# Kernel optimization log

Measured on AMD Instinct MI355X. Metric: run time of the kernel, lower is better.

Reference implementation:

```python
import jax, jax.numpy as jnp
import numpy as np

OUT_FEATURES = 4096
IN_FEATURES = 4096
GROUP_SIZE = 16


def setup_inputs() -> dict:
    key = jax.random.key(0)
    k1, k2, k3, k4 = jax.random.split(key, 4)
    n_groups = OUT_FEATURES * IN_FEATURES // GROUP_SIZE
    x = jax.random.normal(k1, (8, 2048, IN_FEATURES), dtype=jnp.float32)
    weight_q = jax.random.randint(k2, (n_groups, GROUP_SIZE), 0, 16, dtype=jnp.int32).astype(jnp.int8)
    weight_norm = jax.random.uniform(k3, (n_groups, 1), dtype=jnp.float32).astype(jnp.float16)
    bias = jax.random.normal(k4, (OUT_FEATURES,), dtype=jnp.float32)
    return {"x": x, "weight_q": weight_q, "weight_norm": weight_norm, "bias": bias}


def reference(x, weight_q, weight_norm, bias):
    # block dequant: (q/15) * per-group scale, then reshape to [out, in]
    w = (weight_q.astype(jnp.float32) / 15.0) * weight_norm.astype(jnp.float32)
    w = w.reshape(OUT_FEATURES, IN_FEATURES)
    # F.linear: x @ w^T + bias
    return jnp.einsum('bsi,oi->bso', x, w) + bias
```

## Files before the change

### kernel.cpp

```cpp
#include <hip/hip_runtime.h>

#define MDIM 16384
#define NDIM 4096
#define KDIM 4096
#define NT   64

typedef unsigned short u16;
typedef unsigned int   u32;
typedef __attribute__((ext_vector_type(8))) short bh8;
typedef __attribute__((ext_vector_type(4))) float f32x4;
typedef __attribute__((ext_vector_type(4))) int   i32x4;

__device__ __forceinline__ u16 f2bf(float f) {
  u32 u = __builtin_bit_cast(u32, f);
  u = (u + 0x7fffu + ((u >> 16) & 1u)) >> 16;
  return (u16)u;
}

__device__ __forceinline__ void gld16(const void* g, const void* lds) {
  __builtin_amdgcn_global_load_lds((const __attribute__((address_space(1))) u32*)g,
                                   (__attribute__((address_space(3))) u32*)lds, 16, 0, 0);
}

__global__ void cvt_x(const float* __restrict__ x, u16* __restrict__ xb) {
  size_t i = ((size_t)blockIdx.x * 256 + threadIdx.x) * 8;
  f32x4 a = *(const f32x4*)(x + i);
  f32x4 b = *(const f32x4*)(x + i + 4);
  bh8 o;
  o[0] = (short)f2bf(a[0]); o[1] = (short)f2bf(a[1]);
  o[2] = (short)f2bf(a[2]); o[3] = (short)f2bf(a[3]);
  o[4] = (short)f2bf(b[0]); o[5] = (short)f2bf(b[1]);
  o[6] = (short)f2bf(b[2]); o[7] = (short)f2bf(b[3]);
  *(bh8*)(xb + i) = o;
}

__global__ void deq_w(const int* __restrict__ qi, const void* __restrict__ nrm,
                      u16* __restrict__ wb) {
  __shared__ int s_q8, s_n32;
  if (threadIdx.x == 0) {
    int packed = 0;
    for (int t = 0; t < 64; ++t) { unsigned v = (unsigned)qi[t]; if (v > 15u) packed = 1; }
    int n32 = 0;
    const u16* h = (const u16*)nrm;
    for (int t = 0; t < 64; ++t) { u16 b = h[t]; if (b < 0x8000u && b > 0x3C00u) n32 = 1; }
    s_q8 = packed; s_n32 = n32;
  }
  __syncthreads();
  const bool q8 = (s_q8 != 0), n32 = (s_n32 != 0);

  int g = blockIdx.x * 256 + threadIdx.x;
  float s;
  if (n32) s = ((const float*)nrm)[g] * (1.0f / 15.0f);
  else {
    u16 hb = ((const u16*)nrm)[g];
    s = (float)__builtin_bit_cast(_Float16, hb) * (1.0f / 15.0f);
  }
  float q[16];
  if (q8) {
    i32x4 v = *(const i32x4*)((const unsigned char*)qi + (size_t)g * 16);
#pragma unroll
    for (int k = 0; k < 4; ++k) {
      int word = v[k];
      q[k*4+0] = (float)(word & 255);        q[k*4+1] = (float)((word >> 8) & 255);
      q[k*4+2] = (float)((word >> 16) & 255); q[k*4+3] = (float)((word >> 24) & 255);
    }
  } else {
    const i32x4* p = (const i32x4*)(qi + (size_t)g * 16);
#pragma unroll
    for (int k = 0; k < 4; ++k) {
      i32x4 v = p[k];
      q[k*4+0] = (float)v[0]; q[k*4+1] = (float)v[1];
      q[k*4+2] = (float)v[2]; q[k*4+3] = (float)v[3];
    }
  }
  bh8 o0, o1;
#pragma unroll
  for (int j = 0; j < 8; ++j) o0[j] = (short)f2bf(q[j] * s);
#pragma unroll
  for (int j = 0; j < 8; ++j) o1[j] = (short)f2bf(q[8 + j] * s);
  *(bh8*)(wb + (size_t)g * 16) = o0;
  *(bh8*)(wb + (size_t)g * 16 + 8) = o1;
}

__global__ __launch_bounds__(512, 2) void gemm8(const u16* __restrict__ A,
                                                const u16* __restrict__ B,
                                                const float* __restrict__ bias,
                                                float* __restrict__ out) {
  __shared__ u16 lds[65536];
  const int tid = threadIdx.x;
  const int w = tid >> 6, l = tid & 63;
  const int wm = w >> 2, wn = w & 3;

  int bid = blockIdx.x;
  int wg = (bid & 7) * 128 + (bid >> 3);
  const int bm = wg >> 4;
  const int bn = wg & 15;

  const int cs8  = ((l & 7) ^ (l >> 3)) * 8;
  const u16* aSrc = A + (size_t)(bm * 256 + w * 32 + (l >> 3)) * 4096 + cs8;
  const u16* bSrc = B + (size_t)(bn * 256 + w * 32 + (l >> 3)) * 4096 + cs8;

  const int fr  = (l & 15) * 64;
  const int sz0 = ((l >> 4) ^ (l & 7)) * 8;
  const int sz1 = ((4 + (l >> 4)) ^ (l & 7)) * 8;

  f32x4 acc[8][4];
#pragma unroll
  for (int mi = 0; mi < 8; ++mi)
#pragma unroll
    for (int ni = 0; ni < 4; ++ni) acc[mi][ni] = (f32x4){0.f, 0.f, 0.f, 0.f};

  bh8 aX[2][2], aY[2][2];
  bh8 bf_[4][2];

  auto STG = [&](int op, int h, int kt) {
    const u16* s = (op ? bSrc : aSrc) + h * 65536 + kt * 64;
    int d = (op ? 32768 : 0) + ((kt & 1) * 2 + h) * 8192 + w * 1024;
    gld16(s,         &lds[d]);
    gld16(s + 32768, &lds[d + 512]);
  };
  auto RDA = [&](int buf, int mb, bh8 (&aa)[2][2]) {
#pragma unroll
    for (int q = 0; q < 2; ++q) {
      int base = (buf * 2 + q) * 8192 + (wm * 4 + mb) * 1024 + fr;
      aa[q][0] = *(const bh8*)&lds[base + sz0];
      aa[q][1] = *(const bh8*)&lds[base + sz1];
    }
  };
  auto RDB = [&](int buf) {
#pragma unroll
    for (int r = 0; r < 4; ++r) {
      int base = 32768 + (buf * 2 + (r & 1)) * 8192 + (wn * 2 + (r >> 1)) * 1024 + fr;
      bf_[r][0] = *(const bh8*)&lds[base + sz0];
      bf_[r][1] = *(const bh8*)&lds[base + sz1];
    }
  };
  auto MMB = [&](int mb, bh8 (&aa)[2][2]) {
    __builtin_amdgcn_s_setprio(1);
#pragma unroll
    for (int kk = 0; kk < 2; ++kk)
#pragma unroll
      for (int q = 0; q < 2; ++q)
#pragma unroll
        for (int r = 0; r < 4; ++r)
          acc[mb*2+q][r] = __builtin_amdgcn_mfma_f32_16x16x32_bf16(
              aa[q][kk], bf_[r][kk], acc[mb*2+q][r], 0, 0, 0);
    __builtin_amdgcn_s_setprio(0);
  };

#define BAR1 __builtin_amdgcn_s_barrier(); asm volatile("" ::: "memory");
#define BAR2 __builtin_amdgcn_s_barrier();

  STG(1, 0, 0); STG(1, 1, 0); STG(0, 0, 0); STG(0, 1, 0);
  STG(1, 0, 1); STG(1, 1, 1); STG(0, 0, 1); STG(0, 1, 1);
  asm volatile("s_waitcnt vmcnt(8)");
  BAR1;
  RDA(0, 0, aX);

#pragma unroll 1
  for (int i = 0; i < NT / 2 - 1; ++i) {
    const int c = 2 * i + 2, d = 2 * i + 3;
    RDB(0); RDA(0, 1, aY);
    BAR1; MMB(0, aX); BAR2;
    RDA(0, 2, aX); STG(1, 0, c);
    BAR1; MMB(1, aY); BAR2;
    RDA(0, 3, aY); STG(1, 1, c);
    BAR1; MMB(2, aX); BAR2;
    STG(0, 0, c); asm volatile("s_waitcnt vmcnt(6)");
    BAR1; RDA(1, 0, aX); MMB(3, aY); BAR2;
    RDB(1); RDA(1, 1, aY); STG(0, 1, c);
    BAR1; MMB(0, aX); BAR2;
    RDA(1, 2, aX); STG(1, 0, d);
    BAR1; MMB(1, aY); BAR2;
    RDA(1, 3, aY); STG(1, 1, d);
    BAR1; MMB(2, aX); BAR2;
    STG(0, 0, d); STG(0, 1, d); asm volatile("s_waitcnt vmcnt(8)");
    BAR1; RDA(0, 0, aX); MMB(3, aY); BAR2;
  }
  RDB(0); RDA(0, 1, aY);
  BAR1; MMB(0, aX); BAR2;
  RDA(0, 2, aX);
  BAR1; MMB(1, aY); BAR2;
  RDA(0, 3, aY);
  BAR1; MMB(2, aX); BAR2;
  asm volatile("s_waitcnt vmcnt(0)");
  BAR1; RDA(1, 0, aX); MMB(3, aY); BAR2;
  RDB(1); RDA(1, 1, aY);
  BAR1; MMB(0, aX); BAR2;
  RDA(1, 2, aX);
  BAR1; MMB(1, aY); BAR2;
  RDA(1, 3, aY);
  BAR1; MMB(2, aX); BAR2;
  BAR1; MMB(3, aY);
#undef BAR1
#undef BAR2

  const int col0 = bn * 256 + wn * 64 + (l & 15);
  const int row0 = bm * 256 + wm * 128 + (l >> 4) * 4;
#pragma unroll
  for (int ni = 0; ni < 4; ++ni) {
    float bv = bias[col0 + ni * 16];
#pragma unroll
    for (int mi = 0; mi < 8; ++mi) {
      size_t base = (size_t)(row0 + mi * 16) * 4096 + (size_t)(col0 + ni * 16);
#pragma unroll
      for (int rr = 0; rr < 4; ++rr)
        out[base + (size_t)rr * 4096] = acc[mi][ni][rr] + bv;
    }
  }
}

__global__ __launch_bounds__(512, 2) void gemm_fb(const float* __restrict__ Af32,
                                                  const u16* __restrict__ Wbf,
                                                  const float* __restrict__ bias,
                                                  float* __restrict__ out) {
  __shared__ u16 lds[65536];
  const int tid = threadIdx.x;
  const int w = tid >> 6, l = tid & 63;
  const int wm = w >> 2, wn = w & 3;
  int bid = blockIdx.x;
  int wg = (bid & 7) * 128 + (bid >> 3);
  const int bm = wg >> 4, bn = wg & 15;

  int srcOffB[4], srcOffA32[4], dstSwzA[4];
#pragma unroll
  for (int j = 0; j < 4; ++j) {
    int ci = (w * 4 + j) * 64 + l;
    int r = ci >> 3, c = ci & 7;
    int cs = c ^ (r & 7);
    srcOffB[j]   = (bn * 256 + r) * 4096 + cs * 8;
    srcOffA32[j] = (bm * 256 + r) * 4096 + c * 8;
    dstSwzA[j]   = r * 64 + cs * 8;
  }
  const int ar = wm * 128 + (l & 15);
  const int br = wn * 64 + (l & 15);
  const int swz0 = (((l >> 4) + 0) ^ (l & 7)) * 8;
  const int swz1 = (((l >> 4) + 4) ^ (l & 7)) * 8;
  const int aoff0 = ar * 64 + swz0, aoff1 = ar * 64 + swz1;
  const int boff0 = 32768 + br * 64 + swz0, boff1 = 32768 + br * 64 + swz1;

  f32x4 acc[8][4];
#pragma unroll
  for (int mi = 0; mi < 8; ++mi)
#pragma unroll
    for (int ni = 0; ni < 4; ++ni) acc[mi][ni] = (f32x4){0.f, 0.f, 0.f, 0.f};

  auto STAGE = [&](int bufb, int kt) {
    const int kof = kt * 64;
#pragma unroll
    for (int j = 0; j < 4; ++j) {
      gld16(Wbf + srcOffB[j] + kof, &lds[32768 + bufb * 16384 + (w * 4 + j) * 512]);
      const float* p = Af32 + srcOffA32[j] + kof;
      f32x4 v0 = *(const f32x4*)p;
      f32x4 v1 = *(const f32x4*)(p + 4);
      bh8 o;
      o[0] = (short)f2bf(v0[0]); o[1] = (short)f2bf(v0[1]);
      o[2] = (short)f2bf(v0[2]); o[3] = (short)f2bf(v0[3]);
      o[4] = (short)f2bf(v1[0]); o[5] = (short)f2bf(v1[1]);
      o[6] = (short)f2bf(v1[2]); o[7] = (short)f2bf(v1[3]);
      *(bh8*)&lds[bufb * 16384 + dstSwzA[j]] = o;
    }
  };
  auto COMPUTE = [&](int bufb) {
    const int ab = bufb * 16384;
#pragma unroll
    for (int kk = 0; kk < 2; ++kk) {
      const int ao = ab + (kk ? aoff1 : aoff0);
      const int bo = ab + (kk ? boff1 : boff0);
      bh8 afr[8], bfr[4];
#pragma unroll
      for (int mi = 0; mi < 8; ++mi) afr[mi] = *(const bh8*)&lds[ao + mi * 1024];
#pragma unroll
      for (int ni = 0; ni < 4; ++ni) bfr[ni] = *(const bh8*)&lds[bo + ni * 1024];
#pragma unroll
      for (int mi = 0; mi < 8; ++mi)
#pragma unroll
        for (int ni = 0; ni < 4; ++ni)
          acc[mi][ni] = __builtin_amdgcn_mfma_f32_16x16x32_bf16(afr[mi], bfr[ni],
                                                                acc[mi][ni], 0, 0, 0);
    }
  };

  int buf = 0;
  STAGE(0, 0);
  __syncthreads();
  for (int kt = 0; kt < NT - 1; ++kt) {
    STAGE(buf ^ 1, kt + 1);
    COMPUTE(buf);
    __syncthreads();
    buf ^= 1;
  }
  COMPUTE(buf);

  const int col0 = bn * 256 + wn * 64 + (l & 15);
  const int row0 = bm * 256 + wm * 128 + (l >> 4) * 4;
#pragma unroll
  for (int ni = 0; ni < 4; ++ni) {
    float bv = bias[col0 + ni * 16];
#pragma unroll
    for (int mi = 0; mi < 8; ++mi) {
      size_t base = (size_t)(row0 + mi * 16) * 4096 + (size_t)(col0 + ni * 16);
#pragma unroll
      for (int rr = 0; rr < 4; ++rr)
        out[base + (size_t)rr * 4096] = acc[mi][ni][rr] + bv;
    }
  }
}

extern "C" void kernel_launch(void* const* d_in, const int* in_sizes, int n_in,
                              void* d_out, int out_size, void* d_ws, size_t ws_size,
                              hipStream_t stream) {
  const float* x    = (const float*)d_in[0];
  const int*   wq   = (const int*)d_in[1];
  const void*  wn   = d_in[2];
  const float* bias = (const float*)d_in[3];
  float*       out  = (float*)d_out;

  const size_t needA = (size_t)MDIM * KDIM * 2;
  const size_t needW = (size_t)NDIM * KDIM * 2;

  if (ws_size >= needA + needW) {
    u16* xbf = (u16*)d_ws;
    u16* wbf = (u16*)((char*)d_ws + needA);
    cvt_x<<<dim3(32768), dim3(256), 0, stream>>>(x, xbf);
    deq_w<<<dim3(4096), dim3(256), 0, stream>>>(wq, wn, wbf);
    gemm8<<<dim3(1024), dim3(512), 0, stream>>>(xbf, wbf, bias, out);
  } else if (ws_size >= needW) {
    u16* wbf = (u16*)d_ws;
    deq_w<<<dim3(4096), dim3(256), 0, stream>>>(wq, wn, wbf);
    gemm_fb<<<dim3(1024), dim3(512), 0, stream>>>(x, wbf, bias, out);
  }
}
```

Baseline: 544.7 us.

## Switch main GEMM to 32x32x16 MFMA with fragment-ordered LDS layout

Replaces the 16x16x32 bf16 MFMA tiles with 32x32x16 MFMA. The staging now copies global memory into LDS in an order that matches each lane's fragment, so each lane reads contiguous 16-byte chunks and the XOR swizzle is no longer needed. The accumulator layout and the epilogue store mapping change to fit the 32x32 output fragment. The aim is fewer MFMA issues and LDS reads for the same work. In exchange, the new LDS layout may bring bank conflicts, global loads become narrower strided 16-element chunks, and the output stores are less coalesced.

```diff
diff --git a/kernel.cpp b/kernel.cpp
--- a/kernel.cpp
+++ b/kernel.cpp
@@ -9,6 +9,7 @@
 typedef unsigned int   u32;
 typedef __attribute__((ext_vector_type(8))) short bh8;
 typedef __attribute__((ext_vector_type(4))) float f32x4;
+typedef __attribute__((ext_vector_type(16))) float f32x16;
 typedef __attribute__((ext_vector_type(4))) int   i32x4;
 
 __device__ __forceinline__ u16 f2bf(float f) {
@@ -96,60 +97,55 @@
   const int bm = wg >> 4;
   const int bn = wg & 15;
 
-  const int cs8  = ((l & 7) ^ (l >> 3)) * 8;
-  const u16* aSrc = A + (size_t)(bm * 256 + w * 32 + (l >> 3)) * 4096 + cs8;
-  const u16* bSrc = B + (size_t)(bn * 256 + w * 32 + (l >> 3)) * 4096 + cs8;
-
-  const int fr  = (l & 15) * 64;
-  const int sz0 = ((l >> 4) ^ (l & 7)) * 8;
-  const int sz1 = ((4 + (l >> 4)) ^ (l & 7)) * 8;
-
-  f32x4 acc[8][4];
-#pragma unroll
-  for (int mi = 0; mi < 8; ++mi)
-#pragma unroll
-    for (int ni = 0; ni < 4; ++ni) acc[mi][ni] = (f32x4){0.f, 0.f, 0.f, 0.f};
-
-  bh8 aX[2][2], aY[2][2];
-  bh8 bf_[4][2];
-
-  auto STG = [&](int op, int h, int kt) {
-    const u16* s = (op ? bSrc : aSrc) + h * 65536 + kt * 64;
-    int d = (op ? 32768 : 0) + ((kt & 1) * 2 + h) * 8192 + w * 1024;
-    gld16(s,         &lds[d]);
-    gld16(s + 32768, &lds[d + 512]);
-  };
-  auto RDA = [&](int buf, int mb, bh8 (&aa)[2][2]) {
-#pragma unroll
-    for (int q = 0; q < 2; ++q) {
-      int base = (buf * 2 + q) * 8192 + (wm * 4 + mb) * 1024 + fr;
-      aa[q][0] = *(const bh8*)&lds[base + sz0];
-      aa[q][1] = *(const bh8*)&lds[base + sz1];
-    }
+  const u16* aSrcF = A + (size_t)(bm * 256 + (l & 31)) * 4096 + (l >> 5) * 8;
+  const u16* bSrcF = B + (size_t)(bn * 256 + (l & 31)) * 4096 + (l >> 5) * 8;
+
+  f32x16 acc[4][2];
+#pragma unroll
+  for (int mi = 0; mi < 4; ++mi)
+#pragma unroll
+    for (int ni = 0; ni < 2; ++ni)
+#pragma unroll
+      for (int r = 0; r < 16; ++r) acc[mi][ni][r] = 0.f;
+
+  bh8 aX[4], aY[4];
+  bh8 bf_[2][4];
+
+  auto STG = [&](int op, int h, int t) {
+    const int f0 = h * 16 + w * 2;
+    const int mb = f0 >> 2, s = f0 & 3;
+    const u16* src = (op ? bSrcF : aSrcF) + mb * 131072 + s * 16 + t * 64;
+    const int d = (op ? 32768 : 0) + (t & 1) * 16384 + f0 * 512;
+    gld16(src,      &lds[d]);
+    gld16(src + 16, &lds[d + 512]);
+  };
+  auto RDA = [&](int buf, int mbl, bh8 (&aa)[4]) {
+    const int base = buf * 16384 + (wm * 4 + mbl) * 2048 + l * 8;
+#pragma unroll
+    for (int s = 0; s < 4; ++s) aa[s] = *(const bh8*)&lds[base + s * 512];
   };
   auto RDB = [&](int buf) {
 #pragma unroll
-    for (int r = 0; r < 4; ++r) {
-      int base = 32768 + (buf * 2 + (r & 1)) * 8192 + (wn * 2 + (r >> 1)) * 1024 + fr;
-      bf_[r][0] = *(const bh8*)&lds[base + sz0];
-      bf_[r][1] = *(const bh8*)&lds[base + sz1];
-    }
-  };
-  auto MMB = [&](int mb, bh8 (&aa)[2][2]) {
+    for (int nbl = 0; nbl < 2; ++nbl) {
+      const int base = 32768 + buf * 16384 + (wn * 2 + nbl) * 2048 + l * 8;
+#pragma unroll
+      for (int s = 0; s < 4; ++s) bf_[nbl][s] = *(const bh8*)&lds[base + s * 512];
+    }
+  };
+  auto MMB = [&](int mbl, bh8 (&aa)[4]) {
     __builtin_amdgcn_s_setprio(1);
 #pragma unroll
-    for (int kk = 0; kk < 2; ++kk)
-#pragma unroll
-      for (int q = 0; q < 2; ++q)
-#pragma unroll
-        for (int r = 0; r < 4; ++r)
-          acc[mb*2+q][r] = __builtin_amdgcn_mfma_f32_16x16x32_bf16(
-              aa[q][kk], bf_[r][kk], acc[mb*2+q][r], 0, 0, 0);
+    for (int s = 0; s < 4; ++s)
+#pragma unroll
+      for (int nbl = 0; nbl < 2; ++nbl)
+        acc[mbl][nbl] = __builtin_amdgcn_mfma_f32_32x32x16_bf16(
+            aa[s], bf_[nbl][s], acc[mbl][nbl], 0, 0, 0);
     __builtin_amdgcn_s_setprio(0);
   };
 
-#define BAR1 __builtin_amdgcn_s_barrier(); asm volatile("" ::: "memory");
-#define BAR2 __builtin_amdgcn_s_barrier();
+#define BAR1 asm volatile("" ::: "memory"); __builtin_amdgcn_s_barrier(); \
+             asm volatile("" ::: "memory");
+#define BAR2 asm volatile("" ::: "memory"); __builtin_amdgcn_s_barrier();
 
   STG(1, 0, 0); STG(1, 1, 0); STG(0, 0, 0); STG(0, 1, 0);
   STG(1, 0, 1); STG(1, 1, 1); STG(0, 0, 1); STG(0, 1, 1);
@@ -195,17 +191,18 @@
 #undef BAR1
 #undef BAR2
 
-  const int col0 = bn * 256 + wn * 64 + (l & 15);
-  const int row0 = bm * 256 + wm * 128 + (l >> 4) * 4;
-#pragma unroll
-  for (int ni = 0; ni < 4; ++ni) {
-    float bv = bias[col0 + ni * 16];
-#pragma unroll
-    for (int mi = 0; mi < 8; ++mi) {
-      size_t base = (size_t)(row0 + mi * 16) * 4096 + (size_t)(col0 + ni * 16);
-#pragma unroll
-      for (int rr = 0; rr < 4; ++rr)
-        out[base + (size_t)rr * 4096] = acc[mi][ni][rr] + bv;
+  const int colb = bn * 256 + wn * 64 + (l & 31);
+  const int rowb = bm * 256 + wm * 128 + 4 * (l >> 5);
+#pragma unroll
+  for (int nbl = 0; nbl < 2; ++nbl) {
+    float bv = bias[colb + nbl * 32];
+#pragma unroll
+    for (int mbl = 0; mbl < 4; ++mbl) {
+#pragma unroll
+      for (int r = 0; r < 16; ++r) {
+        int row = rowb + mbl * 32 + (r & 3) + 8 * (r >> 2);
+        out[(size_t)row * 4096 + colb + nbl * 32] = acc[mbl][nbl][r] + bv;
+      }
     }
   }
 }
```

New measurement: 659.6 us. 21.1% more time.
